# Kernel optimization log

Hardware: AMD Instinct MI355X
Metric: run time of the kernel (lower is better)

The kernel has to match this reference:

```python
import jax, jax.numpy as jnp
import numpy as np
import math

EPS = float(np.finfo(np.float32).eps)
POWER = 4.0  # init power=4


def cube_face_uv(d):
    # OpenGL cube-map face selection: faces +x,-x,+y,-y,+z,-z -> 0..5
    x, y, z = d[:, 0], d[:, 1], d[:, 2]
    ax, ay, az = jnp.abs(x), jnp.abs(y), jnp.abs(z)
    is_x = (ax >= ay) & (ax >= az)
    is_y = (~is_x) & (ay >= az)
    ma = jnp.maximum(ax, jnp.maximum(ay, az))
    face = jnp.where(is_x, jnp.where(x > 0, 0, 1),
           jnp.where(is_y, jnp.where(y > 0, 2, 3), jnp.where(z > 0, 4, 5)))
    sc = jnp.where(is_x, jnp.where(x > 0, -z, z),
         jnp.where(is_y, x, jnp.where(z > 0, x, -x)))
    tc = jnp.where(is_x, -y, jnp.where(is_y, jnp.where(y > 0, z, -z), -y))
    s = 0.5 * (sc / ma + 1.0)
    t = 0.5 * (tc / ma + 1.0)
    return face.astype(jnp.int32), s, t


def bilinear(tex, face, s, t):
    # tex: [6,R,R,3]; clamp-to-edge bilinear at texel centers (i+0.5)/R
    R = tex.shape[1]
    u = s * R - 0.5
    v = t * R - 0.5
    u0 = jnp.floor(u); v0 = jnp.floor(v)
    fu = (u - u0)[:, None]; fv = (v - v0)[:, None]
    u0i = jnp.clip(u0.astype(jnp.int32), 0, R - 1)
    u1i = jnp.clip(u0.astype(jnp.int32) + 1, 0, R - 1)
    v0i = jnp.clip(v0.astype(jnp.int32), 0, R - 1)
    v1i = jnp.clip(v0.astype(jnp.int32) + 1, 0, R - 1)
    c00 = tex[face, v0i, u0i]; c01 = tex[face, v0i, u1i]
    c10 = tex[face, v1i, u0i]; c11 = tex[face, v1i, u1i]
    return (c00 * (1 - fu) + c01 * fu) * (1 - fv) + (c10 * (1 - fu) + c11 * fu) * fv


def setup_inputs() -> dict:
    key = jax.random.key(0)
    k1, k2, k3 = jax.random.split(key, 3)
    B, R = 1048576, 512
    viewdirs = jax.random.normal(k1, (B, 3), dtype=jnp.float32)
    viewdirs = viewdirs / (jnp.linalg.norm(viewdirs, axis=-1, keepdims=True) + 1e-8)
    saSample = jax.random.normal(k2, (B, 1), dtype=jnp.float32)
    # learned cubemap (init_val=-2 plus small noise so gradients are non-trivial)
    bg_mat = -2.0 + 0.1 * jax.random.normal(k3, (6, R, R, 3), dtype=jnp.float32)
    return {
        'viewdirs': viewdirs,
        'saSample': saSample,
        'bg_mat': bg_mat,
        'brightness': jnp.float32(0.0),
        'mul': jnp.float32(1.0),
        'mipbias': jnp.float32(0.5),
    }


def reference(viewdirs, saSample, bg_mat, brightness, mul, mipbias):
    R = bg_mat.shape[1]
    n_mips = int(math.log2(R)) + 1  # 10 for R=512
    # box-filter mip pyramid (as nvdiffrast auto-generates)
    pyr = [bg_mat]
    for _ in range(n_mips - 1):
        tex = pyr[-1]; r = tex.shape[1]
        pyr.append(tex.reshape(6, r // 2, 2, r // 2, 2, 3).mean(axis=(2, 4)))
    # sa2mip (mipnoise = 0)
    ainf = jnp.max(jnp.abs(viewdirs), axis=-1)            # ||u||_inf
    distortion = (1.0 / ainf)[:, None]                    # [B,1]
    saTexel = distortion / R / R
    mip = (saSample - jnp.log(jnp.clip(saTexel, EPS))) / math.log(POWER) / 2 + mipbias
    mip = jnp.clip(mip[:, 0], 0.0, n_mips - 1.0)          # [B]
    face, s, t = cube_face_uv(viewdirs)
    samples = jnp.stack([bilinear(p, face, s, t) for p in pyr], axis=0)  # [L,B,3]
    m0 = jnp.floor(mip).astype(jnp.int32)
    m1 = jnp.minimum(m0 + 1, n_mips - 1)
    frac = (mip - m0)[:, None]
    B = viewdirs.shape[0]
    lo = jnp.take_along_axis(samples, jnp.broadcast_to(m0[None, :, None], (1, B, 3)), axis=0)[0]
    hi = jnp.take_along_axis(samples, jnp.broadcast_to(m1[None, :, None], (1, B, 3)), axis=0)[0]
    sumemb = lo * (1 - frac) + hi * frac                  # single level -> sum is just this
    # activation 'identity': exp(brightness.clip(-1,2) + mul*x).clip(0.01, 1000)
    x = jnp.clip(brightness, -1.0, 2.0) + mul * sumemb
    return jnp.clip(jnp.exp(x), 0.01, 1000.0)
```

## Files before the change

### kernel.cpp

```cpp
#include <hip/hip_runtime.h>
#include <math.h>


#define BASE_R 512
#define N_MIPS 10

__device__ __host__ __forceinline__ size_t mip_off(int m) {
    return (size_t)6 * (262144u - (1u << (2 * (10 - m))));
}

__global__ __launch_bounds__(256) void pyramid_fused_kernel(
    const float* __restrict__ bg, float* __restrict__ ws) {
    __shared__ float bufA[64 * 64 * 3];
    __shared__ float bufB[32 * 32 * 3];

    const int tid = threadIdx.x;
    const int blk = blockIdx.x;
    const int tileX = blk & 7;
    const int tileY = (blk >> 3) & 7;
    const int f = blk >> 6;

    const size_t faceBase = (size_t)f * (512 * 512 * 3);
    for (int i = tid; i < 64 * 48; i += 256) {
        int row = i / 48;
        int col4 = i % 48;
        const float4 v = *reinterpret_cast<const float4*>(
            bg + faceBase + (size_t)(tileY * 64 + row) * 1536 + tileX * 192 + col4 * 4);
        *reinterpret_cast<float4*>(&bufA[row * 192 + col4 * 4]) = v;
    }
    __syncthreads();

    float* src = bufA;
    float* dst = bufB;
    int rs = 64;
#pragma unroll
    for (int L = 1; L <= 6; ++L) {
        const int rd = rs >> 1;
        const int r = BASE_R >> L;
        float* gl = ws + mip_off(L) + (size_t)f * r * r * 3;
        const int y0 = tileY * rd;
        const int x0 = tileX * rd;
        const int n = rd * rd * 3;
        for (int i = tid; i < n; i += 256) {
            int c = i % 3;
            int t = i / 3;
            int x = t % rd;
            int y = t / rd;
            const float* p0 = src + ((2 * y) * rs + 2 * x) * 3 + c;
            const float* p1 = p0 + rs * 3;
            float m = (p0[0] + p0[3] + p1[0] + p1[3]) * 0.25f;
            dst[i] = m;
            gl[((size_t)(y0 + y) * r + (x0 + x)) * 3 + c] = m;
        }
        __syncthreads();
        float* tmp = src; src = dst; dst = tmp;
        rs = rd;
    }
}

__global__ __launch_bounds__(256) void pyramid_tail_kernel(float* __restrict__ ws) {
    __shared__ float l6[1152];
    __shared__ float l7[288];
    __shared__ float l8[72];
    const int tid = threadIdx.x;

    const float* g6 = ws + mip_off(6);
    for (int i = tid; i < 1152; i += 256) l6[i] = g6[i];
    __syncthreads();

    float* g7 = ws + mip_off(7);
    for (int i = tid; i < 288; i += 256) {
        int c = i % 3, t = i / 3;
        int x = t % 4, y = (t / 4) % 4, f = t / 16;
        const float* p0 = l6 + ((f * 8 + 2 * y) * 8 + 2 * x) * 3 + c;
        const float* p1 = p0 + 24;
        float m = (p0[0] + p0[3] + p1[0] + p1[3]) * 0.25f;
        l7[i] = m;
        g7[i] = m;
    }
    __syncthreads();

    float* g8 = ws + mip_off(8);
    for (int i = tid; i < 72; i += 256) {
        int c = i % 3, t = i / 3;
        int x = t % 2, y = (t / 2) % 2, f = t / 4;
        const float* p0 = l7 + ((f * 4 + 2 * y) * 4 + 2 * x) * 3 + c;
        const float* p1 = p0 + 12;
        float m = (p0[0] + p0[3] + p1[0] + p1[3]) * 0.25f;
        l8[i] = m;
        g8[i] = m;
    }
    __syncthreads();

    float* g9 = ws + mip_off(9);
    for (int i = tid; i < 18; i += 256) {
        int c = i % 3, f = i / 3;
        float m = (l8[f * 12 + c] + l8[f * 12 + 3 + c] +
                   l8[f * 12 + 6 + c] + l8[f * 12 + 9 + c]) * 0.25f;
        g9[i] = m;
    }
}

__device__ __forceinline__ const float* mip_base(const float* __restrict__ bg,
                                                 const float* __restrict__ ws,
                                                 int m) {
    if (m == 0) return bg;
    return ws + mip_off(m);
}

__device__ __forceinline__ void sample_mip(const float* __restrict__ tex, int Rm,
                                           int face, float s, float t,
                                           float out3[3]) {
    float u = s * (float)Rm - 0.5f;
    float v = t * (float)Rm - 0.5f;
    float u0 = floorf(u);
    float v0 = floorf(v);
    float fu = u - u0;
    float fv = v - v0;
    int u0i = min(max((int)u0, 0), Rm - 1);
    int u1i = min(max((int)u0 + 1, 0), Rm - 1);
    int v0i = min(max((int)v0, 0), Rm - 1);
    int v1i = min(max((int)v0 + 1, 0), Rm - 1);
    const float* r0 = tex + ((size_t)(face * Rm + v0i) * Rm) * 3;
    const float* r1 = tex + ((size_t)(face * Rm + v1i) * Rm) * 3;
    const float* p00 = r0 + (size_t)u0i * 3;
    const float* p01 = r0 + (size_t)u1i * 3;
    const float* p10 = r1 + (size_t)u0i * 3;
    const float* p11 = r1 + (size_t)u1i * 3;
#pragma unroll
    for (int c = 0; c < 3; ++c) {
        float top = p00[c] * (1.0f - fu) + p01[c] * fu;
        float bot = p10[c] * (1.0f - fu) + p11[c] * fu;
        out3[c] = top * (1.0f - fv) + bot * fv;
    }
}

__global__ __launch_bounds__(256) void cubemap_sample_kernel(
    const float* __restrict__ vd, const float* __restrict__ sa,
    const float* __restrict__ bg, const float* __restrict__ ws,
    float* __restrict__ out, int B,
    const float* __restrict__ p_brightness,
    const float* __restrict__ p_mul,
    const float* __restrict__ p_mipbias) {
    int i = blockIdx.x * blockDim.x + threadIdx.x;
    if (i >= B) return;

    float x = vd[3 * i + 0];
    float y = vd[3 * i + 1];
    float z = vd[3 * i + 2];
    float ax = fabsf(x), ay = fabsf(y), az = fabsf(z);
    float ma = fmaxf(ax, fmaxf(ay, az));

    int face;
    float sc, tc;
    if (ax >= ay && ax >= az) {
        face = (x > 0.0f) ? 0 : 1;
        sc = (x > 0.0f) ? -z : z;
        tc = -y;
    } else if (ay >= az) {
        face = (y > 0.0f) ? 2 : 3;
        sc = x;
        tc = (y > 0.0f) ? z : -z;
    } else {
        face = (z > 0.0f) ? 4 : 5;
        sc = (z > 0.0f) ? x : -x;
        tc = -y;
    }
    float s = 0.5f * (sc / ma + 1.0f);
    float t = 0.5f * (tc / ma + 1.0f);

    float distortion = 1.0f / ma;
    float saTexel = distortion * (1.0f / 262144.0f);
    const float EPSF = 1.1920928955078125e-07f;
    const float LOG4 = 1.3862943611198906f;
    float mip = (sa[i] - logf(fmaxf(saTexel, EPSF))) / LOG4 * 0.5f + p_mipbias[0];
    mip = fminf(fmaxf(mip, 0.0f), (float)(N_MIPS - 1));

    int m0 = (int)floorf(mip);
    int m1 = min(m0 + 1, N_MIPS - 1);
    float frac = mip - (float)m0;

    float lo[3], hi[3];
    sample_mip(mip_base(bg, ws, m0), BASE_R >> m0, face, s, t, lo);
    sample_mip(mip_base(bg, ws, m1), BASE_R >> m1, face, s, t, hi);

    float bb = fminf(fmaxf(p_brightness[0], -1.0f), 2.0f);
    float mulv = p_mul[0];
#pragma unroll
    for (int c = 0; c < 3; ++c) {
        float xv = bb + mulv * (lo[c] * (1.0f - frac) + hi[c] * frac);
        float e = expf(xv);
        out[3 * i + c] = fminf(fmaxf(e, 0.01f), 1000.0f);
    }
}

extern "C" void kernel_launch(void* const* d_in, const int* in_sizes, int n_in,
                              void* d_out, int out_size, void* d_ws, size_t ws_size,
                              hipStream_t stream) {
    const float* viewdirs = (const float*)d_in[0];
    const float* saSample = (const float*)d_in[1];
    const float* bg_mat = (const float*)d_in[2];
    const float* brightness = (const float*)d_in[3];
    const float* mul = (const float*)d_in[4];
    const float* mipbias = (const float*)d_in[5];
    float* out = (float*)d_out;
    float* ws = (float*)d_ws;

    int B = in_sizes[1];

    pyramid_fused_kernel<<<6 * 8 * 8, 256, 0, stream>>>(bg_mat, ws);
    pyramid_tail_kernel<<<1, 256, 0, stream>>>(ws);

    int blocks = (B + 255) / 256;
    cubemap_sample_kernel<<<blocks, 256, 0, stream>>>(
        viewdirs, saSample, bg_mat, ws, out, B, brightness, mul, mipbias);
}
```

Baseline: 33.88 us.

## Store mip pyramid levels as padded float4 texels for vectorized gathers

Mip levels 1-9 in the workspace now use an RGBA-padded float4 layout, so each bilinear corner fetch in the sampler is one 16-byte load instead of three scalar loads. The pyramid kernels are restructured so each thread computes all three channels of a texel and writes one float4. The sampler splits into a path where both levels come from the workspace, with all eight corner loads issued together, and a level-0 path that uses a noinline scalar sampler on the original texture. The cost is a third more workspace traffic for the pyramid writes, and the noinline call may add overhead.

```diff
diff --git a/kernel.cpp b/kernel.cpp
--- a/kernel.cpp
+++ b/kernel.cpp
@@ -5,8 +5,8 @@
 #define BASE_R 512
 #define N_MIPS 10
 
-__device__ __host__ __forceinline__ size_t mip_off(int m) {
-    return (size_t)6 * (262144u - (1u << (2 * (10 - m))));
+__device__ __forceinline__ size_t mip_off4(int m) {
+    return (size_t)8 * (262144u - (1u << (2 * (10 - m))));
 }
 
 __global__ __launch_bounds__(256) void pyramid_fused_kernel(
@@ -37,20 +37,22 @@
     for (int L = 1; L <= 6; ++L) {
         const int rd = rs >> 1;
         const int r = BASE_R >> L;
-        float* gl = ws + mip_off(L) + (size_t)f * r * r * 3;
+        float4* gl4 = reinterpret_cast<float4*>(ws + mip_off4(L)) + (size_t)f * r * r;
         const int y0 = tileY * rd;
         const int x0 = tileX * rd;
-        const int n = rd * rd * 3;
+        const int n = rd * rd;
         for (int i = tid; i < n; i += 256) {
-            int c = i % 3;
-            int t = i / 3;
-            int x = t % rd;
-            int y = t / rd;
-            const float* p0 = src + ((2 * y) * rs + 2 * x) * 3 + c;
+            int x = i % rd;
+            int y = i / rd;
+            const float* p0 = src + ((2 * y) * rs + 2 * x) * 3;
             const float* p1 = p0 + rs * 3;
-            float m = (p0[0] + p0[3] + p1[0] + p1[3]) * 0.25f;
-            dst[i] = m;
-            gl[((size_t)(y0 + y) * r + (x0 + x)) * 3 + c] = m;
+            float m0 = (p0[0] + p0[3] + p1[0] + p1[3]) * 0.25f;
+            float m1 = (p0[1] + p0[4] + p1[1] + p1[4]) * 0.25f;
+            float m2 = (p0[2] + p0[5] + p1[2] + p1[5]) * 0.25f;
+            dst[i * 3 + 0] = m0;
+            dst[i * 3 + 1] = m1;
+            dst[i * 3 + 2] = m2;
+            gl4[(size_t)(y0 + y) * r + (x0 + x)] = make_float4(m0, m1, m2, 0.0f);
         }
         __syncthreads();
         float* tmp = src; src = dst; dst = tmp;
@@ -64,74 +66,94 @@
     __shared__ float l8[72];
     const int tid = threadIdx.x;
 
-    const float* g6 = ws + mip_off(6);
-    for (int i = tid; i < 1152; i += 256) l6[i] = g6[i];
-    __syncthreads();
-
-    float* g7 = ws + mip_off(7);
-    for (int i = tid; i < 288; i += 256) {
-        int c = i % 3, t = i / 3;
-        int x = t % 4, y = (t / 4) % 4, f = t / 16;
-        const float* p0 = l6 + ((f * 8 + 2 * y) * 8 + 2 * x) * 3 + c;
+    const float4* g6 = reinterpret_cast<const float4*>(ws + mip_off4(6));
+    for (int i = tid; i < 384; i += 256) {
+        float4 v = g6[i];
+        l6[i * 3 + 0] = v.x; l6[i * 3 + 1] = v.y; l6[i * 3 + 2] = v.z;
+    }
+    __syncthreads();
+
+    float4* g7 = reinterpret_cast<float4*>(ws + mip_off4(7));
+    for (int i = tid; i < 96; i += 256) {
+        int x = i % 4, y = (i / 4) % 4, f = i / 16;
+        const float* p0 = l6 + ((f * 8 + 2 * y) * 8 + 2 * x) * 3;
         const float* p1 = p0 + 24;
-        float m = (p0[0] + p0[3] + p1[0] + p1[3]) * 0.25f;
-        l7[i] = m;
-        g7[i] = m;
-    }
-    __syncthreads();
-
-    float* g8 = ws + mip_off(8);
-    for (int i = tid; i < 72; i += 256) {
-        int c = i % 3, t = i / 3;
-        int x = t % 2, y = (t / 2) % 2, f = t / 4;
-        const float* p0 = l7 + ((f * 4 + 2 * y) * 4 + 2 * x) * 3 + c;
+        float m0 = (p0[0] + p0[3] + p1[0] + p1[3]) * 0.25f;
+        float m1 = (p0[1] + p0[4] + p1[1] + p1[4]) * 0.25f;
+        float m2 = (p0[2] + p0[5] + p1[2] + p1[5]) * 0.25f;
+        l7[i * 3 + 0] = m0; l7[i * 3 + 1] = m1; l7[i * 3 + 2] = m2;
+        g7[i] = make_float4(m0, m1, m2, 0.0f);
+    }
+    __syncthreads();
+
+    float4* g8 = reinterpret_cast<float4*>(ws + mip_off4(8));
+    for (int i = tid; i < 24; i += 256) {
+        int x = i % 2, y = (i / 2) % 2, f = i / 4;
+        const float* p0 = l7 + ((f * 4 + 2 * y) * 4 + 2 * x) * 3;
         const float* p1 = p0 + 12;
-        float m = (p0[0] + p0[3] + p1[0] + p1[3]) * 0.25f;
-        l8[i] = m;
-        g8[i] = m;
-    }
-    __syncthreads();
-
-    float* g9 = ws + mip_off(9);
-    for (int i = tid; i < 18; i += 256) {
-        int c = i % 3, f = i / 3;
-        float m = (l8[f * 12 + c] + l8[f * 12 + 3 + c] +
-                   l8[f * 12 + 6 + c] + l8[f * 12 + 9 + c]) * 0.25f;
-        g9[i] = m;
-    }
-}
-
-__device__ __forceinline__ const float* mip_base(const float* __restrict__ bg,
-                                                 const float* __restrict__ ws,
-                                                 int m) {
-    if (m == 0) return bg;
-    return ws + mip_off(m);
-}
-
-__device__ __forceinline__ void sample_mip(const float* __restrict__ tex, int Rm,
-                                           int face, float s, float t,
-                                           float out3[3]) {
+        float m0 = (p0[0] + p0[3] + p1[0] + p1[3]) * 0.25f;
+        float m1 = (p0[1] + p0[4] + p1[1] + p1[4]) * 0.25f;
+        float m2 = (p0[2] + p0[5] + p1[2] + p1[5]) * 0.25f;
+        l8[i * 3 + 0] = m0; l8[i * 3 + 1] = m1; l8[i * 3 + 2] = m2;
+        g8[i] = make_float4(m0, m1, m2, 0.0f);
+    }
+    __syncthreads();
+
+    float4* g9 = reinterpret_cast<float4*>(ws + mip_off4(9));
+    for (int i = tid; i < 6; i += 256) {
+        const float* p = l8 + i * 12;
+        float m0 = (p[0] + p[3] + p[6] + p[9]) * 0.25f;
+        float m1 = (p[1] + p[4] + p[7] + p[10]) * 0.25f;
+        float m2 = (p[2] + p[5] + p[8] + p[11]) * 0.25f;
+        g9[i] = make_float4(m0, m1, m2, 0.0f);
+    }
+}
+
+__device__ __forceinline__ void corner_idx(int Rm, int face, float s, float t,
+                                           int& i00, int& i01, int& i10, int& i11,
+                                           float& fu, float& fv) {
     float u = s * (float)Rm - 0.5f;
     float v = t * (float)Rm - 0.5f;
     float u0 = floorf(u);
     float v0 = floorf(v);
-    float fu = u - u0;
-    float fv = v - v0;
+    fu = u - u0;
+    fv = v - v0;
     int u0i = min(max((int)u0, 0), Rm - 1);
     int u1i = min(max((int)u0 + 1, 0), Rm - 1);
     int v0i = min(max((int)v0, 0), Rm - 1);
     int v1i = min(max((int)v0 + 1, 0), Rm - 1);
-    const float* r0 = tex + ((size_t)(face * Rm + v0i) * Rm) * 3;
-    const float* r1 = tex + ((size_t)(face * Rm + v1i) * Rm) * 3;
-    const float* p00 = r0 + (size_t)u0i * 3;
-    const float* p01 = r0 + (size_t)u1i * 3;
-    const float* p10 = r1 + (size_t)u0i * 3;
-    const float* p11 = r1 + (size_t)u1i * 3;
+    int fb = face * Rm;
+    i00 = (fb + v0i) * Rm + u0i;
+    i01 = (fb + v0i) * Rm + u1i;
+    i10 = (fb + v1i) * Rm + u0i;
+    i11 = (fb + v1i) * Rm + u1i;
+}
+
+__device__ __forceinline__ void blend4(float4 c00, float4 c01, float4 c10, float4 c11,
+                                       float fu, float fv, float o[3]) {
+    o[0] = (c00.x * (1.0f - fu) + c01.x * fu) * (1.0f - fv) +
+           (c10.x * (1.0f - fu) + c11.x * fu) * fv;
+    o[1] = (c00.y * (1.0f - fu) + c01.y * fu) * (1.0f - fv) +
+           (c10.y * (1.0f - fu) + c11.y * fu) * fv;
+    o[2] = (c00.z * (1.0f - fu) + c01.z * fu) * (1.0f - fv) +
+           (c10.z * (1.0f - fu) + c11.z * fu) * fv;
+}
+
+__device__ __noinline__ void sample_bg(const float* __restrict__ bg, int face,
+                                       float s, float t, float o[3]) {
+    const int Rm = BASE_R;
+    int i00, i01, i10, i11;
+    float fu, fv;
+    corner_idx(Rm, face, s, t, i00, i01, i10, i11, fu, fv);
+    const float* p00 = bg + (size_t)i00 * 3;
+    const float* p01 = bg + (size_t)i01 * 3;
+    const float* p10 = bg + (size_t)i10 * 3;
+    const float* p11 = bg + (size_t)i11 * 3;
 #pragma unroll
     for (int c = 0; c < 3; ++c) {
         float top = p00[c] * (1.0f - fu) + p01[c] * fu;
         float bot = p10[c] * (1.0f - fu) + p11[c] * fu;
-        out3[c] = top * (1.0f - fv) + bot * fv;
+        o[c] = top * (1.0f - fv) + bot * fv;
     }
 }
 
@@ -181,8 +203,27 @@
     float frac = mip - (float)m0;
 
     float lo[3], hi[3];
-    sample_mip(mip_base(bg, ws, m0), BASE_R >> m0, face, s, t, lo);
-    sample_mip(mip_base(bg, ws, m1), BASE_R >> m1, face, s, t, hi);
+    if (m0 >= 1) {
+        const float4* ta = reinterpret_cast<const float4*>(ws + mip_off4(m0));
+        const float4* tb = reinterpret_cast<const float4*>(ws + mip_off4(m1));
+        int Ra = BASE_R >> m0, Rb = BASE_R >> m1;
+        int a00, a01, a10, a11, b00, b01, b10, b11;
+        float afu, afv, bfu, bfv;
+        corner_idx(Ra, face, s, t, a00, a01, a10, a11, afu, afv);
+        corner_idx(Rb, face, s, t, b00, b01, b10, b11, bfu, bfv);
+        float4 A00 = ta[a00], A01 = ta[a01], A10 = ta[a10], A11 = ta[a11];
+        float4 B00 = tb[b00], B01 = tb[b01], B10 = tb[b10], B11 = tb[b11];
+        blend4(A00, A01, A10, A11, afu, afv, lo);
+        blend4(B00, B01, B10, B11, bfu, bfv, hi);
+    } else {
+        sample_bg(bg, face, s, t, lo);
+        const float4* tb = reinterpret_cast<const float4*>(ws + mip_off4(1));
+        int Rb = BASE_R >> 1;
+        int b00, b01, b10, b11;
+        float bfu, bfv;
+        corner_idx(Rb, face, s, t, b00, b01, b10, b11, bfu, bfv);
+        blend4(tb[b00], tb[b01], tb[b10], tb[b11], bfu, bfv, hi);
+    }
 
     float bb = fminf(fmaxf(p_brightness[0], -1.0f), 2.0f);
     float mulv = p_mul[0];
```

Measured after the change: 33.20 us. 1.02x faster.
